# Kernel optimization log

Measured on AMD Instinct MI355X. Metric: run time of the kernel, lower is better.

## Reference

```python
import jax, jax.numpy as jnp
import numpy as np
import math
from itertools import combinations_with_replacement

BN_EPS = 1e-5


def _gen_exponents(d, degree):
    num_poly = math.comb(degree + d, d)
    exps = np.zeros((num_poly, d), dtype=np.int32)
    i = 0
    for total_degree in range(degree + 1):
        for combo in combinations_with_replacement(range(d), total_degree):
            for var in combo:
                exps[i, var] += 1
            i += 1
    return exps[1:]  # drop the constant (all-zero) multi-index


def setup_inputs() -> dict:
    key = jax.random.key(0)
    ks = jax.random.split(key, 12)
    d, degree = 3, 15
    B, N = 32, 2048
    exponents = jnp.asarray(_gen_exponents(d, degree))  # (M=815, 3) int32
    M = exponents.shape[0]
    # points in (-0.9, 0.9) so acos and its gradient are well-defined
    x = (jax.random.uniform(ks[0], (B, d, N), dtype=jnp.float32) * 1.8 - 0.9)

    def lin(k, din, dout):
        kw, kb = jax.random.split(k)
        scale = 1.0 / np.sqrt(din)
        W = jax.random.uniform(kw, (din, dout), jnp.float32, -scale, scale)
        b = jax.random.uniform(kb, (dout,), jnp.float32, -scale, scale)
        return W, b

    dims = [M, 512, 256, 128]
    inp = {"x": x, "exponents": exponents}
    for i in range(3):
        W, b = lin(ks[1 + i], dims[i], dims[i + 1])
        h = dims[i + 1]
        inp[f"W{i+1}"], inp[f"b{i+1}"] = W, b
        inp[f"g{i+1}"] = jnp.ones((h,), jnp.float32)   # BN weight
        inp[f"be{i+1}"] = jnp.zeros((h,), jnp.float32)  # BN bias
        inp[f"rm{i+1}"] = jnp.zeros((h,), jnp.float32)  # BN running mean
        inp[f"rv{i+1}"] = jnp.ones((h,), jnp.float32)   # BN running var
    W4, b4 = lin(ks[10], 128, 40)
    inp["W4"], inp["b4"] = W4, b4
    return inp


def _moments_chebyshev(x, exponents):
    # x: (B, d, N) -> X: (B, N, d)
    X = jnp.transpose(x, (0, 2, 1))
    ac = jnp.arccos(X)                              # (B, N, d)
    e = exponents.astype(ac.dtype)                  # (M, d)
    # T_{e_j}(X_j) = cos(e_j * acos(X_j)); product over d, mean over N
    cheb = jnp.cos(e[None, None, :, :] * ac[:, :, None, :])  # (B, N, M, d)
    return cheb.prod(axis=-1).sum(axis=1) / X.shape[1]       # (B, M)


def _lin_bn_relu(h, W, b, g, be, rm, rv):
    h = h @ W + b
    h = g * (h - rm) / jnp.sqrt(rv + BN_EPS) + be  # BatchNorm1d, eval mode
    return jax.nn.relu(h)


def reference(x, exponents,
              W1, b1, g1, be1, rm1, rv1,
              W2, b2, g2, be2, rm2, rv2,
              W3, b3, g3, be3, rm3, rv3,
              W4, b4):
    feats = _moments_chebyshev(x, exponents)  # (B, 815)
    h = _lin_bn_relu(feats, W1, b1, g1, be1, rm1, rv1)
    h = _lin_bn_relu(h, W2, b2, g2, be2, rm2, rv2)
    h = _lin_bn_relu(h, W3, b3, g3, be3, rm3, rv3)
    return h @ W4 + b4  # (B, 40)
```

## Files before the change

### kernel.cpp

```cpp
#include <hip/hip_runtime.h>
#include <math.h>

#define NPTS   2048
#define BATCH  32
#define M_POLY 815
#define GPB    2
#define NSPLIT 16
#define RSTR   192
#define BN_EPS 1e-5f


__device__ __forceinline__ bool decode_chunk(int ci, int& Lo, int& k0o, int& co, int& qo) {
    int idx = 0, qoff = 0;
    for (int l = 0; l < 16; ++l) {
        const int nb   = (l + 4) >> 2;
        const int cmin = (l == 0) ? 1 : 0;
        const int nc   = 16 - l - cmin;
        for (int kb = 0; kb < nb; ++kb) {
            if (ci < idx + nc) {
                Lo = l; k0o = kb * 4; co = cmin + (ci - idx);
                qo = 32 + qoff + kb * 4;
                return true;
            }
            idx += nc;
        }
        qoff += nb * 4;
    }
    return false;
}

__global__ __launch_bounds__(256) void moments_kernel(
    const float* __restrict__ x,
    float*       __restrict__ part)
{
    __shared__ __align__(16) float P[64 * RSTR];
    const int t  = threadIdx.x;
    const int sb = blockIdx.x;
    const int b  = blockIdx.y;
    const int nn = t & 63;
    const int qq = t >> 6;
    const int sw = 4 * (nn & 7);
    const int base = nn * RSTR;

    int L, k0, c, qoff4;
    decode_chunk(t, L, k0, c, qoff4);
    const bool dual = (t >= 61 && t <= 63);
    int L2 = 0, k02 = 0, c2 = 0, qoff42 = 32;
    if (dual) decode_chunk(256 + (t - 61), L2, k02, c2, qoff42);

    int qx[8], tx[8], q2x[8], t2x[8];
    #pragma unroll
    for (int r = 0; r < 8; ++r) {
        qx[r]  = qoff4  ^ (4 * r);
        tx[r]  = c      ^ (4 * r);
        q2x[r] = qoff42 ^ (4 * r);
        t2x[r] = c2     ^ (4 * r);
    }

    float a[4]  = {0.f, 0.f, 0.f, 0.f};
    float a2[4] = {0.f, 0.f, 0.f, 0.f};
    const float* xb = x + (size_t)b * 3 * NPTS;

    for (int g = 0; g < GPB; ++g) {
        if (g) __syncthreads();
        {
            const int n = (sb * GPB + g) * 64 + nn;
            const float x1 = xb[NPTS + n], x2 = xb[2 * NPTS + n];
            float T1r[16], T2r[16];
            T1r[0] = 1.f; T1r[1] = x1;
            #pragma unroll
            for (int k = 2; k < 16; ++k) T1r[k] = 2.f * x1 * T1r[k-1] - T1r[k-2];
            T2r[0] = 1.f; T2r[1] = x2;
            #pragma unroll
            for (int k = 2; k < 16; ++k) T2r[k] = 2.f * x2 * T2r[k-1] - T2r[k-2];

            #define QVAL(S,E) (((E) <= (S)) ? T1r[((S)-(E)) & 15] * T2r[(E) & 15] : 0.f)
            #define ROWQ(S, QO) { \
                _Pragma("unroll") \
                for (int blk = 0; blk < ((S)+4)/4; ++blk) { \
                    float4 v; \
                    v.x = QVAL(S, 4*blk+0); v.y = QVAL(S, 4*blk+1); \
                    v.z = QVAL(S, 4*blk+2); v.w = QVAL(S, 4*blk+3); \
                    *(float4*)&P[base + ((32 + (QO) + 4*blk) ^ sw)] = v; } }

            if (qq == 0) {
                const float x0 = xb[n];
                float T0r[16];
                T0r[0] = 1.f; T0r[1] = x0;
                #pragma unroll
                for (int k = 2; k < 16; ++k) T0r[k] = 2.f * x0 * T0r[k-1] - T0r[k-2];
                #pragma unroll
                for (int blk = 0; blk < 8; ++blk) {
                    float4 v;
                    v.x = (4*blk+0 < 16) ? T0r[(4*blk+0) & 15] : 0.f;
                    v.y = (4*blk+1 < 16) ? T0r[(4*blk+1) & 15] : 0.f;
                    v.z = (4*blk+2 < 16) ? T0r[(4*blk+2) & 15] : 0.f;
                    v.w = (4*blk+3 < 16) ? T0r[(4*blk+3) & 15] : 0.f;
                    *(float4*)&P[base + ((4*blk) ^ sw)] = v;
                }
                ROWQ(0, 0)  ROWQ(1, 4)  ROWQ(2, 8)  ROWQ(3, 12)
            } else if (qq == 1) {
                ROWQ(4, 16) ROWQ(5, 24) ROWQ(6, 32) ROWQ(7, 40) ROWQ(8, 48)
            } else if (qq == 2) {
                ROWQ(9, 60) ROWQ(10, 72) ROWQ(11, 84) ROWQ(12, 96)
            } else {
                ROWQ(13, 112) ROWQ(14, 128) ROWQ(15, 144)
            }
            #undef ROWQ
            #undef QVAL
        }
        __syncthreads();

        for (int n8 = 0; n8 < 8; ++n8) {
            const float* rp0 = &P[n8 * 8 * RSTR];
            #pragma unroll
            for (int r = 0; r < 8; ++r) {
                const float* rp = rp0 + r * RSTR;
                const float t0v = rp[tx[r]];
                const float4 q = *(const float4*)&rp[qx[r]];
                a[0] = fmaf(t0v, q.x, a[0]);
                a[1] = fmaf(t0v, q.y, a[1]);
                a[2] = fmaf(t0v, q.z, a[2]);
                a[3] = fmaf(t0v, q.w, a[3]);
                if (dual) {
                    const float u0 = rp[t2x[r]];
                    const float4 p2 = *(const float4*)&rp[q2x[r]];
                    a2[0] = fmaf(u0, p2.x, a2[0]);
                    a2[1] = fmaf(u0, p2.y, a2[1]);
                    a2[2] = fmaf(u0, p2.z, a2[2]);
                    a2[3] = fmaf(u0, p2.w, a2[3]);
                }
            }
        }
    }

    float* pb = part + ((size_t)b * NSPLIT + sb) * M_POLY;
    {
        const int D  = c + L;
        const int mb = D * (D + 1) * (D + 2) / 6 - 1 + L * (L + 1) / 2;
        const int nv = (L - k0 + 1 < 4) ? (L - k0 + 1) : 4;
        #pragma unroll
        for (int i = 0; i < 4; ++i)
            if (i < nv) pb[mb + k0 + i] = a[i];
    }
    if (dual) {
        const int D  = c2 + L2;
        const int mb = D * (D + 1) * (D + 2) / 6 - 1 + L2 * (L2 + 1) / 2;
        const int nv = (L2 - k02 + 1 < 4) ? (L2 - k02 + 1) : 4;
        #pragma unroll
        for (int i = 0; i < 4; ++i)
            if (i < nv) pb[mb + k02 + i] = a2[i];
    }
}

__global__ __launch_bounds__(512) void l1_kernel(
    const float* __restrict__ part,
    const float* __restrict__ W1, const float* __restrict__ b1,
    const float* __restrict__ g1, const float* __restrict__ be1,
    const float* __restrict__ rm1, const float* __restrict__ rv1,
    float* __restrict__ h1)
{
    __shared__ float fs[816];
    __shared__ float red[16][32];
    const int t  = threadIdx.x;
    const int og = blockIdx.x;
    const int b  = blockIdx.y;

    {
        float s0 = 0.f;
        #pragma unroll
        for (int sp = 0; sp < NSPLIT; ++sp)
            s0 += part[((size_t)b * NSPLIT + sp) * M_POLY + t];
        fs[t] = s0 * (1.0f / (float)NPTS);
        if (t < 303) {
            float s1 = 0.f;
            #pragma unroll
            for (int sp = 0; sp < NSPLIT; ++sp)
                s1 += part[((size_t)b * NSPLIT + sp) * M_POLY + 512 + t];
            fs[512 + t] = s1 * (1.0f / (float)NPTS);
        }
        if (t == 0) fs[815] = 0.f;
    }
    __syncthreads();

    const int o  = og * 32 + (t & 31);
    const int cg = t >> 5;
    const int kb = cg * 51;
    float acc = 0.f;
    #pragma unroll 8
    for (int kk = 0; kk < 51; ++kk) {
        const int k  = kb + kk;
        const int kr = (k < 815) ? k : 814;
        acc = fmaf(fs[k], W1[(size_t)kr * 512 + o], acc);
    }
    red[cg][t & 31] = acc;
    __syncthreads();

    if (t < 32) {
        float dot = 0.f;
        #pragma unroll
        for (int j = 0; j < 16; ++j) dot += red[j][t];
        const int oo = og * 32 + t;
        const float v = (dot + b1[oo] - rm1[oo]) * g1[oo] * rsqrtf(rv1[oo] + BN_EPS) + be1[oo];
        h1[b * 512 + oo] = v > 0.f ? v : 0.f;
    }
}

__global__ __launch_bounds__(512) void l2_kernel(
    const float* __restrict__ h1,
    const float* __restrict__ W2, const float* __restrict__ b2,
    const float* __restrict__ g2, const float* __restrict__ be2,
    const float* __restrict__ rm2, const float* __restrict__ rv2,
    float* __restrict__ h2)
{
    __shared__ float hs[512];
    __shared__ float red[16][32];
    const int t  = threadIdx.x;
    const int og = blockIdx.x;
    const int b  = blockIdx.y;

    hs[t] = h1[b * 512 + t];
    __syncthreads();

    const int o  = og * 32 + (t & 31);
    const int cg = t >> 5;
    const int kb = cg * 32;
    float acc = 0.f;
    #pragma unroll
    for (int kk = 0; kk < 32; ++kk)
        acc = fmaf(hs[kb + kk], W2[(size_t)(kb + kk) * 256 + o], acc);
    red[cg][t & 31] = acc;
    __syncthreads();

    if (t < 32) {
        float dot = 0.f;
        #pragma unroll
        for (int j = 0; j < 16; ++j) dot += red[j][t];
        const int oo = og * 32 + t;
        const float v = (dot + b2[oo] - rm2[oo]) * g2[oo] * rsqrtf(rv2[oo] + BN_EPS) + be2[oo];
        h2[b * 256 + oo] = v > 0.f ? v : 0.f;
    }
}

__global__ __launch_bounds__(512) void l34_kernel(
    const float* __restrict__ h2,
    const float* __restrict__ W3, const float* __restrict__ b3,
    const float* __restrict__ g3, const float* __restrict__ be3,
    const float* __restrict__ rm3, const float* __restrict__ rv3,
    const float* __restrict__ W4, const float* __restrict__ b4,
    float* __restrict__ out)
{
    __shared__ float hs[256];
    __shared__ float red3[4][128];
    __shared__ float h3s[128];
    __shared__ float red4[8][64];
    const int t = threadIdx.x;
    const int b = blockIdx.x;

    if (t < 256) hs[t] = h2[b * 256 + t];
    __syncthreads();

    {
        const int o  = t & 127;
        const int cg = t >> 7;
        const int kb = cg * 64;
        float acc = 0.f;
        #pragma unroll 8
        for (int kk = 0; kk < 64; ++kk)
            acc = fmaf(hs[kb + kk], W3[(size_t)(kb + kk) * 128 + o], acc);
        red3[cg][o] = acc;
    }
    __syncthreads();
    if (t < 128) {
        float dot = red3[0][t] + red3[1][t] + red3[2][t] + red3[3][t];
        const float v = (dot + b3[t] - rm3[t]) * g3[t] * rsqrtf(rv3[t] + BN_EPS) + be3[t];
        h3s[t] = v > 0.f ? v : 0.f;
    }
    __syncthreads();

    {
        const int o  = t & 63;
        const int om = (o < 40) ? o : 39;
        const int cg = t >> 6;
        const int kb = cg * 16;
        float acc = 0.f;
        #pragma unroll
        for (int kk = 0; kk < 16; ++kk)
            acc = fmaf(h3s[kb + kk], W4[(size_t)(kb + kk) * 40 + om], acc);
        red4[cg][o] = acc;
    }
    __syncthreads();
    if (t < 40) {
        float dot = 0.f;
        #pragma unroll
        for (int j = 0; j < 8; ++j) dot += red4[j][t];
        out[b * 40 + t] = dot + b4[t];
    }
}

extern "C" void kernel_launch(void* const* d_in, const int* in_sizes, int n_in,
                              void* d_out, int out_size, void* d_ws, size_t ws_size,
                              hipStream_t stream) {
    const float* x  = (const float*)d_in[0];
    const float* W1 = (const float*)d_in[2];
    const float* b1 = (const float*)d_in[3];
    const float* g1 = (const float*)d_in[4];
    const float* be1= (const float*)d_in[5];
    const float* rm1= (const float*)d_in[6];
    const float* rv1= (const float*)d_in[7];
    const float* W2 = (const float*)d_in[8];
    const float* b2 = (const float*)d_in[9];
    const float* g2 = (const float*)d_in[10];
    const float* be2= (const float*)d_in[11];
    const float* rm2= (const float*)d_in[12];
    const float* rv2= (const float*)d_in[13];
    const float* W3 = (const float*)d_in[14];
    const float* b3 = (const float*)d_in[15];
    const float* g3 = (const float*)d_in[16];
    const float* be3= (const float*)d_in[17];
    const float* rm3= (const float*)d_in[18];
    const float* rv3= (const float*)d_in[19];
    const float* W4 = (const float*)d_in[20];
    const float* b4 = (const float*)d_in[21];
    float* out = (float*)d_out;

    float* part = (float*)d_ws;
    float* h1   = part + (size_t)BATCH * NSPLIT * M_POLY;
    float* h2   = h1 + (size_t)BATCH * 512;

    moments_kernel<<<dim3(NSPLIT, BATCH), 256, 0, stream>>>(x, part);
    l1_kernel<<<dim3(16, BATCH), 512, 0, stream>>>(part,
        W1, b1, g1, be1, rm1, rv1, h1);
    l2_kernel<<<dim3(8, BATCH), 512, 0, stream>>>(h1,
        W2, b2, g2, be2, rm2, rv2, h2);
    l34_kernel<<<BATCH, 512, 0, stream>>>(h2,
        W3, b3, g3, be3, rm3, rv3, W4, b4, out);
}
```

Before: 33.36 us.

## Transpose T0 into separate LDS region and vectorize T0 loads; widen l1 tiles

The moments kernel moves the x0 Chebyshev values out of the per-point row into a separate rotated, transposed LDS region. Each thread can then load four consecutive points' T0 values with one float4 instead of one scalar read per point, and the row stride shrinks from 192 to 160. The three leftover 'dual' chunks are hardcoded as the c=0 case: plain sums written at fixed offset 799, which removes their T0 loads and multiplies. Separately, l1_kernel now uses 64 outputs per block with 8 K-groups instead of 32 with 16, halving its grid. This trades fewer blocks and a longer serial dot per thread for fewer partial-sum reductions.

```diff
diff --git a/kernel.cpp b/kernel.cpp
--- a/kernel.cpp
+++ b/kernel.cpp
@@ -6,9 +6,9 @@
 #define M_POLY 815
 #define GPB    2
 #define NSPLIT 16
-#define RSTR   192
+#define QSTR   160
+#define T0OFF  10240
 #define BN_EPS 1e-5f
-
 
 __device__ __forceinline__ bool decode_chunk(int ci, int& Lo, int& k0o, int& co, int& qo) {
     int idx = 0, qoff = 0;
@@ -19,7 +19,7 @@
         for (int kb = 0; kb < nb; ++kb) {
             if (ci < idx + nc) {
                 Lo = l; k0o = kb * 4; co = cmin + (ci - idx);
-                qo = 32 + qoff + kb * 4;
+                qo = qoff + kb * 4;
                 return true;
             }
             idx += nc;
@@ -33,28 +33,26 @@
     const float* __restrict__ x,
     float*       __restrict__ part)
 {
-    __shared__ __align__(16) float P[64 * RSTR];
+    __shared__ __align__(16) float P[64 * QSTR + 1024];
     const int t  = threadIdx.x;
     const int sb = blockIdx.x;
     const int b  = blockIdx.y;
     const int nn = t & 63;
     const int qq = t >> 6;
     const int sw = 4 * (nn & 7);
-    const int base = nn * RSTR;
+    const int base = nn * QSTR;
 
     int L, k0, c, qoff4;
     decode_chunk(t, L, k0, c, qoff4);
-    const bool dual = (t >= 61 && t <= 63);
-    int L2 = 0, k02 = 0, c2 = 0, qoff42 = 32;
-    if (dual) decode_chunk(256 + (t - 61), L2, k02, c2, qoff42);
-
-    int qx[8], tx[8], q2x[8], t2x[8];
+    const bool dual = (t >= 253);
+    const int k02   = dual ? 4 * (t - 252) : 4;
+    const int qoff42 = 144 + k02;
+
+    int qx[8], q2x[8];
     #pragma unroll
     for (int r = 0; r < 8; ++r) {
         qx[r]  = qoff4  ^ (4 * r);
-        tx[r]  = c      ^ (4 * r);
         q2x[r] = qoff42 ^ (4 * r);
-        t2x[r] = c2     ^ (4 * r);
     }
 
     float a[4]  = {0.f, 0.f, 0.f, 0.f};
@@ -74,14 +72,14 @@
             #pragma unroll
             for (int k = 2; k < 16; ++k) T2r[k] = 2.f * x2 * T2r[k-1] - T2r[k-2];
 
-            #define QVAL(S,E) (((E) <= (S)) ? T1r[((S)-(E)) & 15] * T2r[(E) & 15] : 0.f)
-            #define ROWQ(S, QO) { \
+            #define QVAL(SS,E) (((E) <= (SS)) ? T1r[((SS)-(E)) & 15] * T2r[(E) & 15] : 0.f)
+            #define ROWQ(SS, QO) { \
                 _Pragma("unroll") \
-                for (int blk = 0; blk < ((S)+4)/4; ++blk) { \
+                for (int blk2 = 0; blk2 < ((SS)+4)/4; ++blk2) { \
                     float4 v; \
-                    v.x = QVAL(S, 4*blk+0); v.y = QVAL(S, 4*blk+1); \
-                    v.z = QVAL(S, 4*blk+2); v.w = QVAL(S, 4*blk+3); \
-                    *(float4*)&P[base + ((32 + (QO) + 4*blk) ^ sw)] = v; } }
+                    v.x = QVAL(SS, 4*blk2+0); v.y = QVAL(SS, 4*blk2+1); \
+                    v.z = QVAL(SS, 4*blk2+2); v.w = QVAL(SS, 4*blk2+3); \
+                    *(float4*)&P[base + (((QO) + 4*blk2) ^ sw)] = v; } }
 
             if (qq == 0) {
                 const float x0 = xb[n];
@@ -90,14 +88,8 @@
                 #pragma unroll
                 for (int k = 2; k < 16; ++k) T0r[k] = 2.f * x0 * T0r[k-1] - T0r[k-2];
                 #pragma unroll
-                for (int blk = 0; blk < 8; ++blk) {
-                    float4 v;
-                    v.x = (4*blk+0 < 16) ? T0r[(4*blk+0) & 15] : 0.f;
-                    v.y = (4*blk+1 < 16) ? T0r[(4*blk+1) & 15] : 0.f;
-                    v.z = (4*blk+2 < 16) ? T0r[(4*blk+2) & 15] : 0.f;
-                    v.w = (4*blk+3 < 16) ? T0r[(4*blk+3) & 15] : 0.f;
-                    *(float4*)&P[base + ((4*blk) ^ sw)] = v;
-                }
+                for (int cc = 0; cc < 16; ++cc)
+                    P[T0OFF + cc * 64 + ((nn + 4 * cc) & 63)] = T0r[cc];
                 ROWQ(0, 0)  ROWQ(1, 4)  ROWQ(2, 8)  ROWQ(3, 12)
             } else if (qq == 1) {
                 ROWQ(4, 16) ROWQ(5, 24) ROWQ(6, 32) ROWQ(7, 40) ROWQ(8, 48)
@@ -111,24 +103,24 @@
         }
         __syncthreads();
 
-        for (int n8 = 0; n8 < 8; ++n8) {
-            const float* rp0 = &P[n8 * 8 * RSTR];
+        #pragma unroll 4
+        for (int q4 = 0; q4 < 16; ++q4) {
+            const int np0 = q4 * 4;
+            const float4 t0q =
+                *(const float4*)&P[T0OFF + c * 64 + ((np0 + 4 * c) & 63)];
             #pragma unroll
-            for (int r = 0; r < 8; ++r) {
-                const float* rp = rp0 + r * RSTR;
-                const float t0v = rp[tx[r]];
-                const float4 q = *(const float4*)&rp[qx[r]];
-                a[0] = fmaf(t0v, q.x, a[0]);
-                a[1] = fmaf(t0v, q.y, a[1]);
-                a[2] = fmaf(t0v, q.z, a[2]);
-                a[3] = fmaf(t0v, q.w, a[3]);
+            for (int i = 0; i < 4; ++i) {
+                const int np = np0 + i;
+                const float* rp = &P[np * QSTR];
+                const float  t0v = ((const float*)&t0q)[i];
+                const float4 qv = *(const float4*)&rp[qx[np & 7]];
+                a[0] = fmaf(t0v, qv.x, a[0]);
+                a[1] = fmaf(t0v, qv.y, a[1]);
+                a[2] = fmaf(t0v, qv.z, a[2]);
+                a[3] = fmaf(t0v, qv.w, a[3]);
                 if (dual) {
-                    const float u0 = rp[t2x[r]];
-                    const float4 p2 = *(const float4*)&rp[q2x[r]];
-                    a2[0] = fmaf(u0, p2.x, a2[0]);
-                    a2[1] = fmaf(u0, p2.y, a2[1]);
-                    a2[2] = fmaf(u0, p2.z, a2[2]);
-                    a2[3] = fmaf(u0, p2.w, a2[3]);
+                    const float4 p2 = *(const float4*)&rp[q2x[np & 7]];
+                    a2[0] += p2.x; a2[1] += p2.y; a2[2] += p2.z; a2[3] += p2.w;
                 }
             }
         }
@@ -144,12 +136,10 @@
             if (i < nv) pb[mb + k0 + i] = a[i];
     }
     if (dual) {
-        const int D  = c2 + L2;
-        const int mb = D * (D + 1) * (D + 2) / 6 - 1 + L2 * (L2 + 1) / 2;
-        const int nv = (L2 - k02 + 1 < 4) ? (L2 - k02 + 1) : 4;
+        const int mb = 799;
         #pragma unroll
         for (int i = 0; i < 4; ++i)
-            if (i < nv) pb[mb + k02 + i] = a2[i];
+            pb[mb + k02 + i] = a2[i];
     }
 }
 
@@ -161,7 +151,7 @@
     float* __restrict__ h1)
 {
     __shared__ float fs[816];
-    __shared__ float red[16][32];
+    __shared__ float red[8][64];
     const int t  = threadIdx.x;
     const int og = blockIdx.x;
     const int b  = blockIdx.y;
@@ -183,24 +173,24 @@
     }
     __syncthreads();
 
-    const int o  = og * 32 + (t & 31);
-    const int cg = t >> 5;
-    const int kb = cg * 51;
+    const int o  = og * 64 + (t & 63);
+    const int cg = t >> 6;
+    const int kb = cg * 102;
     float acc = 0.f;
-    #pragma unroll 8
-    for (int kk = 0; kk < 51; ++kk) {
+    #pragma unroll 6
+    for (int kk = 0; kk < 102; ++kk) {
         const int k  = kb + kk;
         const int kr = (k < 815) ? k : 814;
         acc = fmaf(fs[k], W1[(size_t)kr * 512 + o], acc);
     }
-    red[cg][t & 31] = acc;
-    __syncthreads();
-
-    if (t < 32) {
+    red[cg][t & 63] = acc;
+    __syncthreads();
+
+    if (t < 64) {
         float dot = 0.f;
         #pragma unroll
-        for (int j = 0; j < 16; ++j) dot += red[j][t];
-        const int oo = og * 32 + t;
+        for (int j = 0; j < 8; ++j) dot += red[j][t];
+        const int oo = og * 64 + t;
         const float v = (dot + b1[oo] - rm1[oo]) * g1[oo] * rsqrtf(rv1[oo] + BN_EPS) + be1[oo];
         h1[b * 512 + oo] = v > 0.f ? v : 0.f;
     }
@@ -272,7 +262,7 @@
     }
     __syncthreads();
     if (t < 128) {
-        float dot = red3[0][t] + red3[1][t] + red3[2][t] + red3[3][t];
+        const float dot = red3[0][t] + red3[1][t] + red3[2][t] + red3[3][t];
         const float v = (dot + b3[t] - rm3[t]) * g3[t] * rsqrtf(rv3[t] + BN_EPS) + be3[t];
         h3s[t] = v > 0.f ? v : 0.f;
     }
@@ -329,7 +319,7 @@
     float* h2   = h1 + (size_t)BATCH * 512;
 
     moments_kernel<<<dim3(NSPLIT, BATCH), 256, 0, stream>>>(x, part);
-    l1_kernel<<<dim3(16, BATCH), 512, 0, stream>>>(part,
+    l1_kernel<<<dim3(8, BATCH), 512, 0, stream>>>(part,
         W1, b1, g1, be1, rm1, rv1, h1);
     l2_kernel<<<dim3(8, BATCH), 512, 0, stream>>>(h1,
         W2, b2, g2, be2, rm2, rv2, h2);
```

After: 32.04 us. 4.0% less time.
